# Kernel optimization log

Measured on AMD Instinct MI355X. Metric: run time of the kernel, lower is better.

Reference implementation:

```python
import jax, jax.numpy as jnp
import numpy as np
import math

B, S, H = 2, 2048, 2048
NH = 16
HD = H // NH  # 128
ROPE_THETA = 10000.0


def setup_inputs() -> dict:
    key = jax.random.key(0)
    kx, kq, kk, kv, ko = jax.random.split(key, 5)
    x = jax.random.normal(kx, (B, S, H), jnp.float32)
    # standard llama RoPE tables: angles[p, j] = p / theta^(2j/HD)
    inv_freq = 1.0 / (ROPE_THETA ** (jnp.arange(0, HD, 2, dtype=jnp.float32) / HD))
    ang = jnp.arange(S, dtype=jnp.float32)[:, None] * inv_freq[None, :]  # [S, HD/2]
    scale = 1.0 / math.sqrt(H)
    return {
        "input_tensor": x,
        "freqs_cos": jnp.cos(ang),
        "freqs_sin": jnp.sin(ang),
        "padding_mask": jnp.ones((B, S), jnp.int32),
        "Wq": jax.random.normal(kq, (H, H), jnp.float32) * scale,
        "Wk": jax.random.normal(kk, (H, H), jnp.float32) * scale,
        "Wv": jax.random.normal(kv, (H, H), jnp.float32) * scale,
        "Wo": jax.random.normal(ko, (H, H), jnp.float32) * scale,
    }


def _apply_rope(t, cos, sin):
    # t: [b, s, h, d]; rotate consecutive pairs (complex multiply)
    b, s, h, d = t.shape
    t2 = t.reshape(b, s, h, d // 2, 2)
    c = cos[None, :, None, :]  # [1, s, 1, d/2]
    sn = sin[None, :, None, :]
    re = t2[..., 0] * c - t2[..., 1] * sn
    im = t2[..., 0] * sn + t2[..., 1] * c
    return jnp.stack([re, im], axis=-1).reshape(b, s, h, d)


def reference(input_tensor, freqs_cos, freqs_sin, padding_mask, Wq, Wk, Wv, Wo):
    b, s, _ = input_tensor.shape
    # torch nn.Linear: y = x @ W.T (weight stored [out, in])
    q = (input_tensor @ Wq.T).reshape(b, s, NH, HD)
    k = (input_tensor @ Wk.T).reshape(b, s, NH, HD)
    v = (input_tensor @ Wv.T).reshape(b, s, NH, HD)
    q = _apply_rope(q, freqs_cos, freqs_sin)
    k = _apply_rope(k, freqs_cos, freqs_sin)
    q = q.transpose(0, 2, 1, 3)  # b h s d
    k = k.transpose(0, 2, 1, 3)
    v = v.transpose(0, 2, 1, 3)
    scores = jnp.einsum('bhsd,bhtd->bhst', q, k) / math.sqrt(HD)
    pad = jnp.where(padding_mask.astype(bool), 0.0, -10000.0).astype(scores.dtype)
    scores = scores + pad[:, None, None, :]
    causal = jnp.where(jnp.tril(jnp.ones((s, s), bool)), 0.0, -1e9).astype(scores.dtype)
    scores = scores + causal[None, None, :, :]
    attn = jax.nn.softmax(scores.astype(jnp.float32), axis=-1).astype(q.dtype)
    out = jnp.einsum('bhst,bhtd->bhsd', attn, v)
    out = out.transpose(0, 2, 1, 3).reshape(b, s, NH * HD)
    return out @ Wo.T
```

## Files before the change

### kernel.cpp

```cpp
#include <hip/hip_runtime.h>
#include <math.h>

#define Bn  2
#define Sn  2048
#define Hn  2048
#define NHn 16
#define HDn 128
#define Mn  (Bn * Sn)
#define Kd  Hn

typedef __attribute__((ext_vector_type(8))) short bf16x8;
typedef __attribute__((ext_vector_type(4))) float fx4;

__device__ __forceinline__ unsigned short f2bf(float f) {
    union { float f; unsigned u; } v; v.f = f;
    unsigned r = v.u + 0x7fffu + ((v.u >> 16) & 1u);
    return (unsigned short)(r >> 16);
}

__device__ __forceinline__ void gload16(const unsigned short* g, unsigned short* l) {
    __builtin_amdgcn_global_load_lds(
        (const __attribute__((address_space(1))) unsigned int*)g,
        (__attribute__((address_space(3))) unsigned int*)l, 16, 0, 0);
}

__global__ __launch_bounds__(256)
void cvt_kernel(const float* __restrict__ src, unsigned short* __restrict__ dst, int n8)
{
    int i = blockIdx.x * 256 + threadIdx.x;
    if (i >= n8) return;
    const float4* s = (const float4*)src + (size_t)i * 2;
    float4 a = s[0], b = s[1];
    bf16x8 o;
    o[0] = (short)f2bf(a.x); o[1] = (short)f2bf(a.y);
    o[2] = (short)f2bf(a.z); o[3] = (short)f2bf(a.w);
    o[4] = (short)f2bf(b.x); o[5] = (short)f2bf(b.y);
    o[6] = (short)f2bf(b.z); o[7] = (short)f2bf(b.w);
    *(bf16x8*)(dst + (size_t)i * 8) = o;
}

__global__ __launch_bounds__(256)
void cvt4_kernel(const float* __restrict__ w0, const float* __restrict__ w1,
                 const float* __restrict__ w2, const float* __restrict__ w3,
                 unsigned short* __restrict__ d0, unsigned short* __restrict__ d1,
                 unsigned short* __restrict__ d2, unsigned short* __restrict__ d3,
                 int n8)
{
    int i = blockIdx.x * 256 + threadIdx.x;
    if (i >= n8) return;
    const float* w = (blockIdx.y == 0) ? w0 : (blockIdx.y == 1) ? w1
                    : (blockIdx.y == 2) ? w2 : w3;
    unsigned short* d = (blockIdx.y == 0) ? d0 : (blockIdx.y == 1) ? d1
                       : (blockIdx.y == 2) ? d2 : d3;
    const float4* s = (const float4*)w + (size_t)i * 2;
    float4 a = s[0], b = s[1];
    bf16x8 o;
    o[0] = (short)f2bf(a.x); o[1] = (short)f2bf(a.y);
    o[2] = (short)f2bf(a.z); o[3] = (short)f2bf(a.w);
    o[4] = (short)f2bf(b.x); o[5] = (short)f2bf(b.y);
    o[6] = (short)f2bf(b.z); o[7] = (short)f2bf(b.w);
    *(bf16x8*)(d + (size_t)i * 8) = o;
}

__device__ __forceinline__ void gemm_mfma(const unsigned short* __restrict__ A,
                                          const unsigned short* __restrict__ W,
                                          int m0, int n0, fx4 acc[4][4],
                                          unsigned short* Asl, unsigned short* Bsl)
{
    const int t = threadIdx.x;
    const int w = t >> 6, lane = t & 63;
    const int wm = w >> 1, wn = w & 1;
    const int lr = lane & 15, lg = lane >> 4;

    const int srow = w * 32 + (lane >> 2);
    const int scol = (lane & 3) * 8;
    const unsigned short* Ag0 = A + (size_t)(m0 + srow) * Kd + scol;
    const unsigned short* Ag1 = Ag0 + (size_t)16 * Kd;
    const unsigned short* Bg0 = W + (size_t)(n0 + srow) * Kd + scol;
    const unsigned short* Bg1 = Bg0 + (size_t)16 * Kd;
    unsigned short* Ad0 = Asl + w * 1024;
    unsigned short* Ad1 = Asl + w * 1024 + 512;
    unsigned short* Bd0 = Bsl + w * 1024;
    unsigned short* Bd1 = Bsl + w * 1024 + 512;

    for (int k0 = 0; k0 < Kd; k0 += 32) {
        __syncthreads();
        gload16(Ag0 + k0, Ad0);
        gload16(Ag1 + k0, Ad1);
        gload16(Bg0 + k0, Bd0);
        gload16(Bg1 + k0, Bd1);
        __syncthreads();

        bf16x8 af[4], bfr[4];
        #pragma unroll
        for (int i = 0; i < 4; ++i)
            af[i] = *(const bf16x8*)(Asl + (wm * 64 + i * 16 + lr) * 32 + lg * 8);
        #pragma unroll
        for (int j = 0; j < 4; ++j)
            bfr[j] = *(const bf16x8*)(Bsl + (wn * 64 + j * 16 + lr) * 32 + lg * 8);
        #pragma unroll
        for (int i = 0; i < 4; ++i)
            #pragma unroll
            for (int j = 0; j < 4; ++j)
                acc[i][j] = __builtin_amdgcn_mfma_f32_16x16x32_bf16(af[i], bfr[j], acc[i][j], 0, 0, 0);
    }
}

__global__ __launch_bounds__(256)
void qkv_kernel(const unsigned short* __restrict__ xb,
                const unsigned short* __restrict__ wq, const unsigned short* __restrict__ wk,
                const unsigned short* __restrict__ wv,
                const float* __restrict__ fcos, const float* __restrict__ fsin,
                unsigned short* __restrict__ qb, unsigned short* __restrict__ kb,
                unsigned short* __restrict__ vtb)
{
    __shared__ unsigned short Asl[128 * 32];
    __shared__ unsigned short Bsl[128 * 32];
    const int mode = blockIdx.z;
    const unsigned short* W = (mode == 0) ? wq : (mode == 1) ? wk : wv;
    const int m0 = blockIdx.x * 128, n0 = blockIdx.y * 128;

    fx4 zero = {0.f, 0.f, 0.f, 0.f};
    fx4 acc[4][4];
    #pragma unroll
    for (int i = 0; i < 4; ++i)
        #pragma unroll
        for (int j = 0; j < 4; ++j) acc[i][j] = zero;

    gemm_mfma(xb, W, m0, n0, acc, Asl, Bsl);

    const int t = threadIdx.x, w = t >> 6, lane = t & 63;
    const int wm = w >> 1, wn = w & 1, lr = lane & 15, lg = lane >> 4;
    const int h = n0 >> 7;
    if (mode < 2) {
        unsigned short* outp = (mode == 0) ? qb : kb;
        #pragma unroll
        for (int i = 0; i < 4; ++i) {
            int mbase = m0 + wm * 64 + i * 16 + lg * 4;
            #pragma unroll
            for (int j = 0; j < 4; ++j) {
                int d = wn * 64 + j * 16 + lr;
                #pragma unroll
                for (int r = 0; r < 4; ++r) {
                    int m = mbase + r, b = m >> 11, s = m & (Sn - 1);
                    float vv = acc[i][j][r];
                    float other = __shfl_xor(vv, 1, 64);
                    float c  = fcos[s * (HDn / 2) + (d >> 1)];
                    float sn = fsin[s * (HDn / 2) + (d >> 1)];
                    float res = (d & 1) ? (other * sn + vv * c) : (vv * c - other * sn);
                    outp[(((size_t)b * NHn + h) * Sn + s) * HDn + d] = f2bf(res);
                }
            }
        }
    } else {
        #pragma unroll
        for (int i = 0; i < 4; ++i) {
            int mbase = m0 + wm * 64 + i * 16 + lg * 4;
            int b = mbase >> 11, s = mbase & (Sn - 1);
            #pragma unroll
            for (int j = 0; j < 4; ++j) {
                int d = wn * 64 + j * 16 + lr;
                ushort4 pk;
                pk.x = f2bf(acc[i][j][0]); pk.y = f2bf(acc[i][j][1]);
                pk.z = f2bf(acc[i][j][2]); pk.w = f2bf(acc[i][j][3]);
                *(ushort4*)(vtb + (((size_t)b * NHn + h) * HDn + d) * Sn + s) = pk;
            }
        }
    }
}

__global__ __launch_bounds__(256)
void oproj_kernel(const unsigned short* __restrict__ attnb,
                  const unsigned short* __restrict__ wob, float* __restrict__ out)
{
    __shared__ unsigned short Asl[128 * 32];
    __shared__ unsigned short Bsl[128 * 32];
    const int m0 = blockIdx.x * 128, n0 = blockIdx.y * 128;
    fx4 zero = {0.f, 0.f, 0.f, 0.f};
    fx4 acc[4][4];
    #pragma unroll
    for (int i = 0; i < 4; ++i)
        #pragma unroll
        for (int j = 0; j < 4; ++j) acc[i][j] = zero;

    gemm_mfma(attnb, wob, m0, n0, acc, Asl, Bsl);

    const int t = threadIdx.x, w = t >> 6, lane = t & 63;
    const int wm = w >> 1, wn = w & 1, lr = lane & 15, lg = lane >> 4;
    #pragma unroll
    for (int i = 0; i < 4; ++i) {
        #pragma unroll
        for (int r = 0; r < 4; ++r) {
            int m = m0 + wm * 64 + i * 16 + lg * 4 + r;
            #pragma unroll
            for (int j = 0; j < 4; ++j)
                out[(size_t)m * Hn + n0 + wn * 64 + j * 16 + lr] = acc[i][j][r];
        }
    }
}

#define KROW 136
#define VROW 72
#define PROW 68

__global__ __launch_bounds__(256)
void attn_kernel(const unsigned short* __restrict__ qb,
                 const unsigned short* __restrict__ kb,
                 const unsigned short* __restrict__ vtb,
                 const int* __restrict__ pmask, unsigned short* __restrict__ attnb)
{
    __shared__ unsigned short Ksl[64 * KROW];
    __shared__ unsigned short Vsl[128 * VROW];
    __shared__ unsigned short Psl[4 * 16 * PROW];

    const int pr = blockIdx.x, h = blockIdx.y, b = blockIdx.z;
    const size_t base = ((size_t)b * NHn + h) * Sn * HDn;
    const unsigned short* Qp = qb + base;
    const unsigned short* Kp = kb + base;
    const unsigned short* Vt = vtb + base;
    const int t = threadIdx.x, w = t >> 6, lane = t & 63;
    const int lr = lane & 15, lg = lane >> 4;
    const float scale = 0.08838834764831845f;
    fx4 zero = {0.f, 0.f, 0.f, 0.f};

    for (int ph = 0; ph < 2; ++ph) {
        const int qt = ph ? (31 - pr) : pr;
        const int q0 = qt * 64;
        const int nt = qt + 1;

        bf16x8 qf[4];
        #pragma unroll
        for (int kf = 0; kf < 4; ++kf)
            qf[kf] = *(const bf16x8*)(Qp + (size_t)(q0 + w * 16 + lr) * HDn + kf * 32 + lg * 8);

        fx4 oacc[8];
        #pragma unroll
        for (int j = 0; j < 8; ++j) oacc[j] = zero;
        float mrow[4] = {-1e30f, -1e30f, -1e30f, -1e30f};
        float lsum[4] = {0.f, 0.f, 0.f, 0.f};

        bf16x8 kreg[4], vreg[4];
        #pragma unroll
        for (int q = 0; q < 4; ++q) {
            int chunk = t + q * 256, row = chunk >> 4, c = chunk & 15;
            kreg[q] = *(const bf16x8*)(Kp + (size_t)row * HDn + c * 8);
        }
        #pragma unroll
        for (int q = 0; q < 4; ++q) {
            int chunk = t + q * 256, row = chunk >> 3, c = chunk & 7;
            vreg[q] = *(const bf16x8*)(Vt + (size_t)row * Sn + c * 8);
        }

        for (int kt = 0; kt < nt; ++kt) {
            const int kv0 = kt * 64;
            __syncthreads();
            #pragma unroll
            for (int q = 0; q < 4; ++q) {
                int chunk = t + q * 256, row = chunk >> 4, c = chunk & 15;
                *(bf16x8*)(Ksl + row * KROW + c * 8) = kreg[q];
            }
            #pragma unroll
            for (int q = 0; q < 4; ++q) {
                int chunk = t + q * 256, row = chunk >> 3, c = chunk & 7;
                *(bf16x8*)(Vsl + row * VROW + c * 8) = vreg[q];
            }
            __syncthreads();
            if (kt + 1 < nt) {
                #pragma unroll
                for (int q = 0; q < 4; ++q) {
                    int chunk = t + q * 256, row = chunk >> 4, c = chunk & 15;
                    kreg[q] = *(const bf16x8*)(Kp + (size_t)(kv0 + 64 + row) * HDn + c * 8);
                }
                #pragma unroll
                for (int q = 0; q < 4; ++q) {
                    int chunk = t + q * 256, row = chunk >> 3, c = chunk & 7;
                    vreg[q] = *(const bf16x8*)(Vt + (size_t)row * Sn + kv0 + 64 + c * 8);
                }
            }

            fx4 sc[4];
            __builtin_amdgcn_s_setprio(1);
            #pragma unroll
            for (int nf = 0; nf < 4; ++nf) {
                fx4 z = zero;
                #pragma unroll
                for (int kf = 0; kf < 4; ++kf) {
                    bf16x8 kfr = *(const bf16x8*)(Ksl + (nf * 16 + lr) * KROW + kf * 32 + lg * 8);
                    z = __builtin_amdgcn_mfma_f32_16x16x32_bf16(qf[kf], kfr, z, 0, 0, 0);
                }
                sc[nf] = z;
            }
            __builtin_amdgcn_s_setprio(0);

            float pmv[4];
            #pragma unroll
            for (int nf = 0; nf < 4; ++nf)
                pmv[nf] = pmask[b * Sn + kv0 + nf * 16 + lr] ? 0.f : -10000.f;
            float tmax[4];
            #pragma unroll
            for (int r = 0; r < 4; ++r) {
                int qrow = q0 + w * 16 + lg * 4 + r;
                float mx = -1e30f;
                #pragma unroll
                for (int nf = 0; nf < 4; ++nf) {
                    int kg = kv0 + nf * 16 + lr;
                    float v = sc[nf][r] * scale + pmv[nf] + ((kg > qrow) ? -1e9f : 0.f);
                    sc[nf][r] = v;
                    mx = fmaxf(mx, v);
                }
                tmax[r] = mx;
            }
            #pragma unroll
            for (int off = 1; off < 16; off <<= 1)
                #pragma unroll
                for (int r = 0; r < 4; ++r)
                    tmax[r] = fmaxf(tmax[r], __shfl_xor(tmax[r], off, 64));
            float grow = 0.f;
            #pragma unroll
            for (int r = 0; r < 4; ++r) grow = fmaxf(grow, tmax[r] - mrow[r]);
            if (__any(grow > 8.f)) {
                #pragma unroll
                for (int r = 0; r < 4; ++r) {
                    float mnew = fmaxf(mrow[r], tmax[r]);
                    float sf = __expf(mrow[r] - mnew);
                    mrow[r] = mnew;
                    lsum[r] *= sf;
                    #pragma unroll
                    for (int j = 0; j < 8; ++j) oacc[j][r] *= sf;
                }
            }
            float psum[4];
            #pragma unroll
            for (int r = 0; r < 4; ++r) {
                float ps = 0.f;
                #pragma unroll
                for (int nf = 0; nf < 4; ++nf) {
                    float p = __expf(sc[nf][r] - mrow[r]);
                    sc[nf][r] = p;
                    ps += p;
                }
                psum[r] = ps;
            }
            #pragma unroll
            for (int off = 1; off < 16; off <<= 1)
                #pragma unroll
                for (int r = 0; r < 4; ++r)
                    psum[r] += __shfl_xor(psum[r], off, 64);
            #pragma unroll
            for (int r = 0; r < 4; ++r) lsum[r] += psum[r];

            unsigned short* Pw = Psl + w * 16 * PROW;
            #pragma unroll
            for (int nf = 0; nf < 4; ++nf)
                #pragma unroll
                for (int r = 0; r < 4; ++r)
                    Pw[(lg * 4 + r) * PROW + nf * 16 + lr] = f2bf(sc[nf][r]);
            __builtin_amdgcn_s_setprio(1);
            #pragma unroll
            for (int kf2 = 0; kf2 < 2; ++kf2) {
                bf16x8 pf = *(const bf16x8*)(Pw + lr * PROW + kf2 * 32 + lg * 8);
                #pragma unroll
                for (int j = 0; j < 8; ++j) {
                    bf16x8 vf = *(const bf16x8*)(Vsl + (j * 16 + lr) * VROW + kf2 * 32 + lg * 8);
                    oacc[j] = __builtin_amdgcn_mfma_f32_16x16x32_bf16(pf, vf, oacc[j], 0, 0, 0);
                }
            }
            __builtin_amdgcn_s_setprio(0);
        }

        #pragma unroll
        for (int j = 0; j < 8; ++j) {
            int d = j * 16 + lr;
            #pragma unroll
            for (int r = 0; r < 4; ++r) {
                int s = q0 + w * 16 + lg * 4 + r;
                attnb[((size_t)b * Sn + s) * Hn + h * HDn + d] = f2bf(oacc[j][r] / lsum[r]);
            }
        }
        __syncthreads();
    }
}

extern "C" void kernel_launch(void* const* d_in, const int* in_sizes, int n_in,
                              void* d_out, int out_size, void* d_ws, size_t ws_size,
                              hipStream_t stream)
{
    const float* x     = (const float*)d_in[0];
    const float* fcos  = (const float*)d_in[1];
    const float* fsin  = (const float*)d_in[2];
    const int*   pmask = (const int*)d_in[3];
    const float* Wq    = (const float*)d_in[4];
    const float* Wk    = (const float*)d_in[5];
    const float* Wv    = (const float*)d_in[6];
    const float* Wo    = (const float*)d_in[7];
    float* out = (float*)d_out;
    (void)in_sizes; (void)n_in; (void)out_size; (void)ws_size;

    const size_t NX = (size_t)Mn * Hn;
    const size_t NW = (size_t)Hn * Hn;
    unsigned short* xb   = (unsigned short*)d_ws;
    unsigned short* wqb  = xb  + NX;
    unsigned short* wkb  = wqb + NW;
    unsigned short* wvb  = wkb + NW;
    unsigned short* wob  = wvb + NW;
    unsigned short* qb   = wob + NW;
    unsigned short* kb   = qb  + NX;
    unsigned short* vtb  = kb  + NX;
    unsigned short* attnb= vtb + NX;

    cvt_kernel<<<dim3((int)(NX / 8 / 256)), 256, 0, stream>>>(x, xb, (int)(NX / 8));
    cvt4_kernel<<<dim3((int)(NW / 8 / 256), 4), 256, 0, stream>>>(
        Wq, Wk, Wv, Wo, wqb, wkb, wvb, wob, (int)(NW / 8));
    qkv_kernel<<<dim3(Mn / 128, Hn / 128, 3), 256, 0, stream>>>(
        xb, wqb, wkb, wvb, fcos, fsin, qb, kb, vtb);
    attn_kernel<<<dim3(16, NHn, Bn), 256, 0, stream>>>(qb, kb, vtb, pmask, attnb);
    oproj_kernel<<<dim3(Mn / 128, Hn / 128), 256, 0, stream>>>(attnb, wob, out);
}
```

Baseline: 442.7 us.

## Rewrite projection GEMMs as 256x256 tiles with double-buffered swizzled LDS pipeline

Replaces the 128x128, K=32 single-buffer GEMM with a 256x256-tile, 512-thread, K=64 double-buffered kernel. It uses XOR-swizzled LDS layout, interleaved async global->LDS staging, and MFMA sub-phases with setprio, applied to both the QKV and output projections. The aim is better data reuse per load, hidden global load latency and fewer LDS bank conflicts. In exchange it needs 128KB of dynamic LDS, more registers for the accumulators, and fewer blocks in flight (a 16x8x3 and 16x8 grid), which can lower occupancy and wave-level load balance.

```diff
diff --git a/kernel.cpp b/kernel.cpp
--- a/kernel.cpp
+++ b/kernel.cpp
@@ -22,6 +22,10 @@
     __builtin_amdgcn_global_load_lds(
         (const __attribute__((address_space(1))) unsigned int*)g,
         (__attribute__((address_space(3))) unsigned int*)l, 16, 0, 0);
+}
+
+__device__ __forceinline__ fx4 mfma16(bf16x8 a, bf16x8 b, fx4 c) {
+    return __builtin_amdgcn_mfma_f32_16x16x32_bf16(a, b, c, 0, 0, 0);
 }
 
 __global__ __launch_bounds__(256)
@@ -62,51 +66,114 @@
     *(bf16x8*)(d + (size_t)i * 8) = o;
 }
 
-__device__ __forceinline__ void gemm_mfma(const unsigned short* __restrict__ A,
-                                          const unsigned short* __restrict__ W,
-                                          int m0, int n0, fx4 acc[4][4],
-                                          unsigned short* Asl, unsigned short* Bsl)
+#define HALF_SH 8192
+#define B_BASE  32768
+
+__device__ __forceinline__ void gemm256(const unsigned short* __restrict__ A,
+                                        const unsigned short* __restrict__ W,
+                                        int m0, int n0, fx4 acc[8][4],
+                                        unsigned short* smem)
 {
     const int t = threadIdx.x;
-    const int w = t >> 6, lane = t & 63;
-    const int wm = w >> 1, wn = w & 1;
+    const int wid = t >> 6, lane = t & 63;
+    const int wm = wid >> 2, wn = wid & 3;
     const int lr = lane & 15, lg = lane >> 4;
-
-    const int srow = w * 32 + (lane >> 2);
-    const int scol = (lane & 3) * 8;
-    const unsigned short* Ag0 = A + (size_t)(m0 + srow) * Kd + scol;
-    const unsigned short* Ag1 = Ag0 + (size_t)16 * Kd;
-    const unsigned short* Bg0 = W + (size_t)(n0 + srow) * Kd + scol;
-    const unsigned short* Bg1 = Bg0 + (size_t)16 * Kd;
-    unsigned short* Ad0 = Asl + w * 1024;
-    unsigned short* Ad1 = Asl + w * 1024 + 512;
-    unsigned short* Bd0 = Bsl + w * 1024;
-    unsigned short* Bd1 = Bsl + w * 1024 + 512;
-
-    for (int k0 = 0; k0 < Kd; k0 += 32) {
-        __syncthreads();
-        gload16(Ag0 + k0, Ad0);
-        gload16(Ag1 + k0, Ad1);
-        gload16(Bg0 + k0, Bd0);
-        gload16(Bg1 + k0, Bd1);
-        __syncthreads();
-
-        bf16x8 af[4], bfr[4];
+    const int swr = ((lr >> 2) & 3) << 4;
+
+    const int row0 = t >> 3,         row1 = (t + 512) >> 3;
+    const int gc0 = ((t & 7) * 8) ^ (((row0 >> 2) & 3) << 4);
+    const int gc1 = ((t & 7) * 8) ^ (((row1 >> 2) & 3) << 4);
+    const unsigned short* Ag[2][2];
+    const unsigned short* Bg[2][2];
+    Ag[0][0] = A + (size_t)(m0 + row0) * Kd + gc0;
+    Ag[0][1] = A + (size_t)(m0 + row1) * Kd + gc1;
+    Ag[1][0] = A + (size_t)(m0 + 128 + row0) * Kd + gc0;
+    Ag[1][1] = A + (size_t)(m0 + 128 + row1) * Kd + gc1;
+    Bg[0][0] = W + (size_t)(n0 + row0) * Kd + gc0;
+    Bg[0][1] = W + (size_t)(n0 + row1) * Kd + gc1;
+    Bg[1][0] = W + (size_t)(n0 + 128 + row0) * Kd + gc0;
+    Bg[1][1] = W + (size_t)(n0 + 128 + row1) * Kd + gc1;
+    const int dst0 = wid * 512;
+    const int dst1 = wid * 512 + 4096;
+
+    bf16x8 aM[4][2], bLo[2][2], bHi[2][2];
+
+    auto STAGE_A = [&](int buf, int koff) {
+        gload16(Ag[0][0] + koff, smem + (buf * 2 + 0) * HALF_SH + dst0);
+        gload16(Ag[0][1] + koff, smem + (buf * 2 + 0) * HALF_SH + dst1);
+        gload16(Ag[1][0] + koff, smem + (buf * 2 + 1) * HALF_SH + dst0);
+        gload16(Ag[1][1] + koff, smem + (buf * 2 + 1) * HALF_SH + dst1);
+    };
+    auto STAGE_B = [&](int buf, int koff) {
+        gload16(Bg[0][0] + koff, smem + B_BASE + (buf * 2 + 0) * HALF_SH + dst0);
+        gload16(Bg[0][1] + koff, smem + B_BASE + (buf * 2 + 0) * HALF_SH + dst1);
+        gload16(Bg[1][0] + koff, smem + B_BASE + (buf * 2 + 1) * HALF_SH + dst0);
+        gload16(Bg[1][1] + koff, smem + B_BASE + (buf * 2 + 1) * HALF_SH + dst1);
+    };
+    auto LDA = [&](int buf, int milo) {
+        const unsigned short* base = smem + (buf * 2 + wm) * HALF_SH;
+        #pragma unroll
+        for (int i = 0; i < 4; ++i) {
+            int rl = (milo + i) * 16 + lr;
+            #pragma unroll
+            for (int kk = 0; kk < 2; ++kk)
+                aM[i][kk] = *(const bf16x8*)(base + rl * 64 + ((kk * 32 + lg * 8) ^ swr));
+        }
+    };
+    auto LDB = [&](int buf, int njlo, bf16x8 (&br)[2][2]) {
+        const unsigned short* base = smem + B_BASE + (buf * 2 + (wn >> 1)) * HALF_SH;
+        #pragma unroll
+        for (int j = 0; j < 2; ++j) {
+            int rl = (wn & 1) * 64 + (njlo + j) * 16 + lr;
+            #pragma unroll
+            for (int kk = 0; kk < 2; ++kk)
+                br[j][kk] = *(const bf16x8*)(base + rl * 64 + ((kk * 32 + lg * 8) ^ swr));
+        }
+    };
+    auto MM = [&](int milo, int njlo, bf16x8 (&br)[2][2]) {
+        __builtin_amdgcn_s_setprio(1);
         #pragma unroll
         for (int i = 0; i < 4; ++i)
-            af[i] = *(const bf16x8*)(Asl + (wm * 64 + i * 16 + lr) * 32 + lg * 8);
-        #pragma unroll
-        for (int j = 0; j < 4; ++j)
-            bfr[j] = *(const bf16x8*)(Bsl + (wn * 64 + j * 16 + lr) * 32 + lg * 8);
-        #pragma unroll
-        for (int i = 0; i < 4; ++i)
-            #pragma unroll
-            for (int j = 0; j < 4; ++j)
-                acc[i][j] = __builtin_amdgcn_mfma_f32_16x16x32_bf16(af[i], bfr[j], acc[i][j], 0, 0, 0);
+            #pragma unroll
+            for (int j = 0; j < 2; ++j)
+                #pragma unroll
+                for (int kk = 0; kk < 2; ++kk)
+                    acc[milo + i][njlo + j] =
+                        mfma16(aM[i][kk], br[j][kk], acc[milo + i][njlo + j]);
+        __builtin_amdgcn_s_setprio(0);
+    };
+
+    STAGE_A(0, 0);
+    STAGE_B(0, 0);
+    asm volatile("s_waitcnt vmcnt(0)" ::: "memory");
+    __builtin_amdgcn_s_barrier();
+
+    const int NT = Kd / 64;
+    for (int tk = 0; tk < NT; ++tk) {
+        const int cur = tk & 1, nxt = cur ^ 1;
+        const int koff = (tk + 1) * 64;
+        if (tk + 1 < NT) STAGE_A(nxt, koff);
+        LDA(cur, 0);
+        LDB(cur, 0, bLo);
+        __builtin_amdgcn_s_barrier();
+        MM(0, 0, bLo);
+        __builtin_amdgcn_s_barrier();
+        if (tk + 1 < NT) STAGE_B(nxt, koff);
+        LDB(cur, 2, bHi);
+        __builtin_amdgcn_s_barrier();
+        MM(0, 2, bHi);
+        __builtin_amdgcn_s_barrier();
+        LDA(cur, 4);
+        __builtin_amdgcn_s_barrier();
+        MM(4, 2, bHi);
+        __builtin_amdgcn_s_barrier();
+        MM(4, 0, bLo);
+        asm volatile("s_waitcnt vmcnt(0)" ::: "memory");
+        __builtin_amdgcn_s_barrier();
     }
 }
 
-__global__ __launch_bounds__(256)
+__global__ __launch_bounds__(512, 2)
 void qkv_kernel(const unsigned short* __restrict__ xb,
                 const unsigned short* __restrict__ wq, const unsigned short* __restrict__ wk,
                 const unsigned short* __restrict__ wv,
@@ -114,87 +181,86 @@
                 unsigned short* __restrict__ qb, unsigned short* __restrict__ kb,
                 unsigned short* __restrict__ vtb)
 {
-    __shared__ unsigned short Asl[128 * 32];
-    __shared__ unsigned short Bsl[128 * 32];
+    extern __shared__ unsigned short smem[];
     const int mode = blockIdx.z;
     const unsigned short* W = (mode == 0) ? wq : (mode == 1) ? wk : wv;
-    const int m0 = blockIdx.x * 128, n0 = blockIdx.y * 128;
+    const int m0 = blockIdx.x * 256, n0 = blockIdx.y * 256;
 
     fx4 zero = {0.f, 0.f, 0.f, 0.f};
-    fx4 acc[4][4];
+    fx4 acc[8][4];
     #pragma unroll
-    for (int i = 0; i < 4; ++i)
+    for (int i = 0; i < 8; ++i)
         #pragma unroll
         for (int j = 0; j < 4; ++j) acc[i][j] = zero;
 
-    gemm_mfma(xb, W, m0, n0, acc, Asl, Bsl);
-
-    const int t = threadIdx.x, w = t >> 6, lane = t & 63;
-    const int wm = w >> 1, wn = w & 1, lr = lane & 15, lg = lane >> 4;
-    const int h = n0 >> 7;
+    gemm256(xb, W, m0, n0, acc, smem);
+
+    const int t = threadIdx.x, wid = t >> 6, lane = t & 63;
+    const int wm = wid >> 2, wn = wid & 3, lr = lane & 15, lg = lane >> 4;
     if (mode < 2) {
         unsigned short* outp = (mode == 0) ? qb : kb;
         #pragma unroll
-        for (int i = 0; i < 4; ++i) {
-            int mbase = m0 + wm * 64 + i * 16 + lg * 4;
-            #pragma unroll
-            for (int j = 0; j < 4; ++j) {
-                int d = wn * 64 + j * 16 + lr;
+        for (int mi = 0; mi < 8; ++mi) {
+            int mbase = m0 + wm * 128 + mi * 16 + lg * 4;
+            #pragma unroll
+            for (int nj = 0; nj < 4; ++nj) {
+                int ncol = n0 + wn * 64 + nj * 16 + lr;
+                int h = ncol >> 7, dh = ncol & 127;
                 #pragma unroll
                 for (int r = 0; r < 4; ++r) {
                     int m = mbase + r, b = m >> 11, s = m & (Sn - 1);
-                    float vv = acc[i][j][r];
+                    float vv = acc[mi][nj][r];
                     float other = __shfl_xor(vv, 1, 64);
-                    float c  = fcos[s * (HDn / 2) + (d >> 1)];
-                    float sn = fsin[s * (HDn / 2) + (d >> 1)];
-                    float res = (d & 1) ? (other * sn + vv * c) : (vv * c - other * sn);
-                    outp[(((size_t)b * NHn + h) * Sn + s) * HDn + d] = f2bf(res);
+                    float c  = fcos[s * (HDn / 2) + (dh >> 1)];
+                    float sn = fsin[s * (HDn / 2) + (dh >> 1)];
+                    float res = (dh & 1) ? (other * sn + vv * c) : (vv * c - other * sn);
+                    outp[(((size_t)b * NHn + h) * Sn + s) * HDn + dh] = f2bf(res);
                 }
             }
         }
     } else {
         #pragma unroll
-        for (int i = 0; i < 4; ++i) {
-            int mbase = m0 + wm * 64 + i * 16 + lg * 4;
+        for (int mi = 0; mi < 8; ++mi) {
+            int mbase = m0 + wm * 128 + mi * 16 + lg * 4;
             int b = mbase >> 11, s = mbase & (Sn - 1);
             #pragma unroll
-            for (int j = 0; j < 4; ++j) {
-                int d = wn * 64 + j * 16 + lr;
+            for (int nj = 0; nj < 4; ++nj) {
+                int ncol = n0 + wn * 64 + nj * 16 + lr;
+                int h = ncol >> 7, dh = ncol & 127;
                 ushort4 pk;
-                pk.x = f2bf(acc[i][j][0]); pk.y = f2bf(acc[i][j][1]);
-                pk.z = f2bf(acc[i][j][2]); pk.w = f2bf(acc[i][j][3]);
-                *(ushort4*)(vtb + (((size_t)b * NHn + h) * HDn + d) * Sn + s) = pk;
+                pk.x = f2bf(acc[mi][nj][0]); pk.y = f2bf(acc[mi][nj][1]);
+                pk.z = f2bf(acc[mi][nj][2]); pk.w = f2bf(acc[mi][nj][3]);
+                *(ushort4*)(vtb + (((size_t)b * NHn + h) * HDn + dh) * Sn + s) = pk;
             }
         }
     }
 }
 
-__global__ __launch_bounds__(256)
+__global__ __launch_bounds__(512, 2)
 void oproj_kernel(const unsigned short* __restrict__ attnb,
                   const unsigned short* __restrict__ wob, float* __restrict__ out)
 {
-    __shared__ unsigned short Asl[128 * 32];
-    __shared__ unsigned short Bsl[128 * 32];
-    const int m0 = blockIdx.x * 128, n0 = blockIdx.y * 128;
+    extern __shared__ unsigned short smem[];
+    const int m0 = blockIdx.x * 256, n0 = blockIdx.y * 256;
     fx4 zero = {0.f, 0.f, 0.f, 0.f};
-    fx4 acc[4][4];
+    fx4 acc[8][4];
     #pragma unroll
-    for (int i = 0; i < 4; ++i)
+    for (int i = 0; i < 8; ++i)
         #pragma unroll
         for (int j = 0; j < 4; ++j) acc[i][j] = zero;
 
-    gemm_mfma(attnb, wob, m0, n0, acc, Asl, Bsl);
-
-    const int t = threadIdx.x, w = t >> 6, lane = t & 63;
-    const int wm = w >> 1, wn = w & 1, lr = lane & 15, lg = lane >> 4;
+    gemm256(attnb, wob, m0, n0, acc, smem);
+
+    const int t = threadIdx.x, wid = t >> 6, lane = t & 63;
+    const int wm = wid >> 2, wn = wid & 3, lr = lane & 15, lg = lane >> 4;
     #pragma unroll
-    for (int i = 0; i < 4; ++i) {
+    for (int mi = 0; mi < 8; ++mi) {
         #pragma unroll
         for (int r = 0; r < 4; ++r) {
-            int m = m0 + wm * 64 + i * 16 + lg * 4 + r;
-            #pragma unroll
-            for (int j = 0; j < 4; ++j)
-                out[(size_t)m * Hn + n0 + wn * 64 + j * 16 + lr] = acc[i][j][r];
+            int m = m0 + wm * 128 + mi * 16 + lg * 4 + r;
+            #pragma unroll
+            for (int nj = 0; nj < 4; ++nj)
+                out[(size_t)m * Hn + n0 + wn * 64 + nj * 16 + lr] = acc[mi][nj][r];
         }
     }
 }
@@ -408,11 +474,17 @@
     unsigned short* vtb  = kb  + NX;
     unsigned short* attnb= vtb + NX;
 
+    const int GEMM_LDS = 131072;
+    hipFuncSetAttribute((const void*)qkv_kernel,
+                        hipFuncAttributeMaxDynamicSharedMemorySize, GEMM_LDS);
+    hipFuncSetAttribute((const void*)oproj_kernel,
+                        hipFuncAttributeMaxDynamicSharedMemorySize, GEMM_LDS);
+
     cvt_kernel<<<dim3((int)(NX / 8 / 256)), 256, 0, stream>>>(x, xb, (int)(NX / 8));
     cvt4_kernel<<<dim3((int)(NW / 8 / 256), 4), 256, 0, stream>>>(
         Wq, Wk, Wv, Wo, wqb, wkb, wvb, wob, (int)(NW / 8));
-    qkv_kernel<<<dim3(Mn / 128, Hn / 128, 3), 256, 0, stream>>>(
+    qkv_kernel<<<dim3(Mn / 256, Hn / 256, 3), 512, GEMM_LDS, stream>>>(
         xb, wqb, wkb, wvb, fcos, fsin, qb, kb, vtb);
     attn_kernel<<<dim3(16, NHn, Bn), 256, 0, stream>>>(qb, kb, vtb, pmask, attnb);
-    oproj_kernel<<<dim3(Mn / 128, Hn / 128), 256, 0, stream>>>(attnb, wob, out);
-}
+    oproj_kernel<<<dim3(Mn / 256, Hn / 256), 512, GEMM_LDS, stream>>>(attnb, wob, out);
+}
```

Measured after the change: 452.4 us. 1.02x slower.
